# Kernel optimization log

Hardware: AMD Instinct MI355X
Metric: run time of the kernel (lower is better)

Reference implementation:

```python
import jax, jax.numpy as jnp
import numpy as np

J = 161          # skeleton joints
V = 131072       # mesh vertices
K = 8            # max skin joints per vertex
B = 8            # batch
P = 7 * J        # 1127 = total pose params == channels
_rs = np.random.RandomState(1)
JOINT_PARENTS = np.concatenate([np.array([-1]), np.array([_rs.randint(0, i) for i in range(1, J)])])

# quaternion layout (x, y, z, w)

def quat_mul(q1, q2):
    x1, y1, z1, w1 = q1[..., 0], q1[..., 1], q1[..., 2], q1[..., 3]
    x2, y2, z2, w2 = q2[..., 0], q2[..., 1], q2[..., 2], q2[..., 3]
    return jnp.stack([
        w1 * x2 + x1 * w2 + y1 * z2 - z1 * y2,
        w1 * y2 - x1 * z2 + y1 * w2 + z1 * x2,
        w1 * z2 + x1 * y2 - y1 * x2 + z1 * w2,
        w1 * w2 - x1 * x2 - y1 * y2 - z1 * z2,
    ], axis=-1)


def quat_rot(q, v):
    qv = q[..., :3]
    t = 2.0 * jnp.cross(qv, v)
    return v + q[..., 3:4] * t + jnp.cross(qv, t)


def quat_invert(q):
    return jnp.concatenate([-q[..., :3], q[..., 3:4]], axis=-1)


def quat_from_xyz(e):
    h = 0.5 * e
    sx, sy, sz = jnp.sin(h[..., 0]), jnp.sin(h[..., 1]), jnp.sin(h[..., 2])
    cx, cy, cz = jnp.cos(h[..., 0]), jnp.cos(h[..., 1]), jnp.cos(h[..., 2])
    return jnp.stack([
        sx * cy * cz + cx * sy * sz,
        cx * sy * cz - sx * cy * sz,
        cx * cy * sz + sx * sy * cz,
        cx * cy * cz - sx * sy * sz,
    ], axis=-1)


def solve_skeleton_state(params, joint_offset, joint_rotation):
    b = params.shape[0]
    jp = params.reshape(b, J, 7)
    lt = jp[..., 0:3] + joint_offset[None]                       # [b,J,3]
    lr = quat_mul(jnp.broadcast_to(joint_rotation[None], (b, J, 4)), quat_from_xyz(jp[..., 3:6]))
    ls = jnp.exp2(jp[..., 6:7])                                  # [b,J,1]
    states = [None] * J
    for i in range(J):                                           # tree FK recurrence (fixed topology)
        p = int(JOINT_PARENTS[i])
        if p < 0:
            states[i] = (lt[:, i], lr[:, i], ls[:, i])
        else:
            pt, pr, ps = states[p]
            gr = quat_mul(pr, lr[:, i])
            gt = quat_rot(pr, lt[:, i] * ps) + pt
            gs = ps * ls[:, i]
            states[i] = (gt, gr, gs)
    return jnp.stack([jnp.concatenate(s, axis=-1) for s in states], axis=1)  # [b,J,8]


def states_to_matrix(bind_state, states):
    br = quat_invert(bind_state[..., 3:7])
    bs = 1.0 / bind_state[..., 7:8]
    bt = quat_rot(br, -bind_state[..., 0:3]) * bs
    tr = quat_mul(states[..., 3:7], br)
    ts = states[..., 7:8] * bs
    tt = quat_rot(states[..., 3:7], bt * states[..., 7:8]) + states[..., 0:3]
    x, y, z, w = tr[..., 0], tr[..., 1], tr[..., 2], tr[..., 3]
    twx, twy, twz = 2.0 * x * w, 2.0 * y * w, 2.0 * z * w
    txx, txy, txz = 2.0 * x * x, 2.0 * y * x, 2.0 * z * x
    tyy, tyz, tzz = 2.0 * y * y, 2.0 * z * y, 2.0 * z * z
    col0 = jnp.stack([1.0 - (tyy + tzz), txy + twz, txz - twy], axis=-1) * ts
    col1 = jnp.stack([txy - twz, 1.0 - (txx + tzz), tyz + twx], axis=-1) * ts
    col2 = jnp.stack([txz + twy, tyz - twx, 1.0 - (txx + tyy)], axis=-1) * ts
    return jnp.stack([col0, col1, col2, tt], axis=-1)            # [b,J,3,4]


def setup_inputs() -> dict:
    key = jax.random.key(0)
    ks = jax.random.split(key, 10)
    transform = 0.01 * jax.random.normal(ks[0], (P, P), dtype=jnp.float32)
    transform_offsets = 0.01 * jax.random.normal(ks[1], (P,), dtype=jnp.float32)
    joint_offset = jax.random.normal(ks[2], (J, 3), dtype=jnp.float32)
    jr = jax.random.normal(ks[3], (J, 4), dtype=jnp.float32)
    joint_rotation = jr / jnp.linalg.norm(jr, axis=-1, keepdims=True)
    global_pose = 0.1 * jax.random.normal(ks[4], (B, 6), dtype=jnp.float32)
    local_pose = 0.1 * jax.random.normal(ks[5], (B, P - 6 - J), dtype=jnp.float32)
    scale = 0.1 * jax.random.normal(ks[6], (B, J), dtype=jnp.float32)
    mesh_vertices = jax.random.normal(ks[7], (V, 3), dtype=jnp.float32)
    sw = jax.random.uniform(ks[8], (V, K), dtype=jnp.float32)
    skin_weights = sw / sw.sum(axis=-1, keepdims=True)
    skin_indices = jax.random.randint(ks[9], (V, K), 0, J, dtype=jnp.int64)
    # bind state = FK of the zero pose (params = transform_offsets), as in __init__
    bind_state = solve_skeleton_state(transform_offsets[None], joint_offset, joint_rotation)
    return dict(global_pose=global_pose, local_pose=local_pose, scale=scale,
                transform=transform, transform_offsets=transform_offsets,
                joint_offset=joint_offset, joint_rotation=joint_rotation,
                bind_state=bind_state, skin_weights=skin_weights,
                mesh_vertices=mesh_vertices, skin_indices=skin_indices)


def reference(global_pose, local_pose, scale, transform, transform_offsets,
              joint_offset, joint_rotation, bind_state, skin_weights,
              mesh_vertices, skin_indices):
    pose = jnp.concatenate([global_pose, local_pose, scale], axis=-1)   # [B,P]
    params = pose @ transform.T + transform_offsets[None]               # ParameterTransform
    states = solve_skeleton_state(params, joint_offset, joint_rotation) # [B,J,8]
    mat = states_to_matrix(bind_state, states)                          # [B,J,3,4]
    b = mat.shape[0]
    gathered = jnp.take(mat, skin_indices.reshape(-1), axis=1).reshape(b, V, K, 3, 4)
    blended = jnp.einsum('bvkij,vk->bvij', gathered, skin_weights)      # [B,V,3,4]
    return jnp.einsum('bvij,vj->bvi', blended[..., :3], mesh_vertices) + blended[..., 3]
```

## Files before the change

kernel.cpp:

```cpp
#include <hip/hip_runtime.h>
#include <hip/hip_fp16.h>
#include <math.h>

#define Jn 161
#define Vn 131072
#define Kn 8
#define Bn 8
#define Pn 1127
#define NLOC 960
#define MATU (Bn*Jn*6)

struct Q  { float x, y, z, w; };
struct F3 { float x, y, z; };

__device__ __forceinline__ F3 cross3(F3 a, F3 b) {
    return F3{ a.y*b.z - a.z*b.y, a.z*b.x - a.x*b.z, a.x*b.y - a.y*b.x };
}
__device__ __forceinline__ Q qmul(Q a, Q b) {
    return Q{ a.w*b.x + a.x*b.w + a.y*b.z - a.z*b.y,
              a.w*b.y - a.x*b.z + a.y*b.w + a.z*b.x,
              a.w*b.z + a.x*b.y - a.y*b.x + a.z*b.w,
              a.w*b.w - a.x*b.x - a.y*b.y - a.z*b.z };
}
__device__ __forceinline__ F3 qrot(Q q, F3 v) {
    F3 qv{ q.x, q.y, q.z };
    F3 t = cross3(qv, v);
    t.x *= 2.f; t.y *= 2.f; t.z *= 2.f;
    F3 c = cross3(qv, t);
    return F3{ v.x + q.w*t.x + c.x, v.y + q.w*t.y + c.y, v.z + q.w*t.z + c.z };
}
__device__ __forceinline__ Q qfromxyz(float ex, float ey, float ez) {
    float sx = sinf(0.5f*ex), cx = cosf(0.5f*ex);
    float sy = sinf(0.5f*ey), cy = cosf(0.5f*ey);
    float sz = sinf(0.5f*ez), cz = cosf(0.5f*ez);
    return Q{ sx*cy*cz + cx*sy*sz,
              cx*sy*cz - sx*cy*sz,
              cx*cy*sz + sx*sy*cz,
              cx*cy*cz - sx*sy*sz };
}

__device__ __forceinline__ unsigned packh2(float a, float b) {
    unsigned lo = (unsigned)__half_as_ushort(__float2half_rn(a));
    unsigned hi = (unsigned)__half_as_ushort(__float2half_rn(b));
    return lo | (hi << 16);
}
__device__ __forceinline__ float2 unpackh2(unsigned u) {
    float2 r;
    r.x = __half2float(__ushort_as_half((unsigned short)(u & 0xFFFFu)));
    r.y = __half2float(__ushort_as_half((unsigned short)(u >> 16)));
    return r;
}

__global__ __launch_bounds__(64) void k_front(
    const float* __restrict__ gp, const float* __restrict__ lp,
    const float* __restrict__ sc, const float* __restrict__ T,
    const float* __restrict__ toff, const float* __restrict__ joff,
    const float* __restrict__ jrot, const float* __restrict__ bind,
    float* __restrict__ params, int* __restrict__ parents)
{
    const int blk  = blockIdx.x;
    const int lane = threadIdx.x;

    if (blk < Jn) {
        const int i = blk;
        if (i == 0) { if (lane == 0) parents[0] = -1; return; }

        Q fx = qfromxyz(toff[i*7+3], toff[i*7+4], toff[i*7+5]);
        Q jr{ jrot[i*4+0], jrot[i*4+1], jrot[i*4+2], jrot[i*4+3] };
        Q lr = qmul(jr, fx);
        const float l0 = toff[i*7+0] + joff[i*3+0];
        const float l1 = toff[i*7+1] + joff[i*3+1];
        const float l2 = toff[i*7+2] + joff[i*3+2];
        const float lsc = exp2f(toff[i*7+6]);

        float bi[8];
        #pragma unroll
        for (int c = 0; c < 8; ++c) bi[c] = bind[i*8+c];

        unsigned best = 0xFFFFFFFFu;
        for (int p = lane; p < i; p += 64) {
            const float* bp = bind + p*8;
            Q  pr{ bp[3], bp[4], bp[5], bp[6] };
            float ps = bp[7];
            Q  gr = qmul(pr, lr);
            F3 gt = qrot(pr, F3{ l0*ps, l1*ps, l2*ps });
            gt.x += bp[0]; gt.y += bp[1]; gt.z += bp[2];
            float gs = ps * lsc;
            float err = 0.f, d;
            d = gr.x - bi[3]; err += d*d;
            d = gr.y - bi[4]; err += d*d;
            d = gr.z - bi[5]; err += d*d;
            d = gr.w - bi[6]; err += d*d;
            d = gt.x - bi[0]; err += d*d;
            d = gt.y - bi[1]; err += d*d;
            d = gt.z - bi[2]; err += d*d;
            d = gs   - bi[7]; err += d*d;
            unsigned pk = (__float_as_uint(err) & 0xFFFFFF00u) | (unsigned)p;
            best = best < pk ? best : pk;
        }
        #pragma unroll
        for (int o = 32; o > 0; o >>= 1) {
            unsigned other = __shfl_xor(best, o, 64);
            best = best < other ? best : other;
        }
        if (lane == 0) parents[i] = (int)(best & 0xFFu);
        return;
    }

    const int p = blk - Jn;
    const float* row = T + (size_t)p * Pn;

    float acc[Bn];
    #pragma unroll
    for (int b = 0; b < Bn; ++b) acc[b] = 0.f;

    for (int q = lane; q < Pn; q += 64) {
        float tv = row[q];
        #pragma unroll
        for (int b = 0; b < Bn; ++b) {
            float pv;
            if (q < 6)            pv = gp[b*6 + q];
            else if (q < 6+NLOC)  pv = lp[b*NLOC + (q-6)];
            else                  pv = sc[b*Jn + (q-6-NLOC)];
            acc[b] = fmaf(tv, pv, acc[b]);
        }
    }
    #pragma unroll
    for (int b = 0; b < Bn; ++b)
        #pragma unroll
        for (int o = 32; o > 0; o >>= 1)
            acc[b] += __shfl_xor(acc[b], o, 64);

    if (lane == 0) {
        float off = toff[p];
        #pragma unroll
        for (int b = 0; b < Bn; ++b)
            params[b*Pn + p] = acc[b] + off;
    }
}

__global__ __launch_bounds__(192) void k_fk(
    const float* __restrict__ params, const float* __restrict__ joff,
    const float* __restrict__ jrot,   const float* __restrict__ bind,
    const int* __restrict__ parents,  unsigned* __restrict__ mat16)
{
    __shared__ float loc[Jn][9];
    __shared__ int   par[Jn];
    const int b   = blockIdx.x;
    const int tid = threadIdx.x;

    if (tid < Jn) {
        const int i = tid;
        par[i] = parents[i];
        const float* jp = params + b*Pn + i*7;
        Q fx = qfromxyz(jp[3], jp[4], jp[5]);
        Q jr{ jrot[i*4+0], jrot[i*4+1], jrot[i*4+2], jrot[i*4+3] };
        Q lr = qmul(jr, fx);
        loc[i][0] = jp[0] + joff[i*3+0];
        loc[i][1] = jp[1] + joff[i*3+1];
        loc[i][2] = jp[2] + joff[i*3+2];
        loc[i][3] = lr.x; loc[i][4] = lr.y; loc[i][5] = lr.z; loc[i][6] = lr.w;
        loc[i][7] = exp2f(jp[6]);
    }
    __syncthreads();

    if (tid < Jn) {
        const int i = tid;
        F3 at{ loc[i][0], loc[i][1], loc[i][2] };
        Q  ar{ loc[i][3], loc[i][4], loc[i][5], loc[i][6] };
        float as = loc[i][7];
        int j = par[i];
        while (j >= 0) {
            Q  lr{ loc[j][3], loc[j][4], loc[j][5], loc[j][6] };
            float ls = loc[j][7];
            F3 nt = qrot(lr, F3{ at.x*ls, at.y*ls, at.z*ls });
            at = F3{ nt.x + loc[j][0], nt.y + loc[j][1], nt.z + loc[j][2] };
            ar = qmul(lr, ar);
            as = ls * as;
            j = par[j];
        }

        const float* bv = bind + i*8;
        Q  br{ -bv[3], -bv[4], -bv[5], bv[6] };
        float bs = 1.f / bv[7];
        F3 btv = qrot(br, F3{ -bv[0], -bv[1], -bv[2] });
        btv.x *= bs; btv.y *= bs; btv.z *= bs;

        Q  tr = qmul(ar, br);
        float ts = as * bs;
        F3 tt = qrot(ar, F3{ btv.x*as, btv.y*as, btv.z*as });
        tt.x += at.x; tt.y += at.y; tt.z += at.z;

        float x = tr.x, y = tr.y, z = tr.z, w = tr.w;
        float twx = 2.f*x*w, twy = 2.f*y*w, twz = 2.f*z*w;
        float txx = 2.f*x*x, txy = 2.f*y*x, txz = 2.f*z*x;
        float tyy = 2.f*y*y, tyz = 2.f*z*y, tzz = 2.f*z*z;

        float m0  = (1.f - (tyy + tzz)) * ts;
        float m1  = (txy - twz) * ts;
        float m2  = (txz + twy) * ts;
        float m3  = tt.x;
        float m4  = (txy + twz) * ts;
        float m5  = (1.f - (txx + tzz)) * ts;
        float m6  = (tyz - twx) * ts;
        float m7  = tt.y;
        float m8  = (txz - twy) * ts;
        float m9  = (tyz + twx) * ts;
        float m10 = (1.f - (txx + tyy)) * ts;
        float m11 = tt.z;

        unsigned* o = mat16 + (size_t)(b*Jn + i) * 6;
        o[0] = packh2(m0,  m1);
        o[1] = packh2(m2,  m3);
        o[2] = packh2(m4,  m5);
        o[3] = packh2(m6,  m7);
        o[4] = packh2(m8,  m9);
        o[5] = packh2(m10, m11);
    }
}

__global__ __launch_bounds__(256) void k_skin(
    const unsigned* __restrict__ mat16, const float* __restrict__ wts,
    const float* __restrict__ verts, const int* __restrict__ idx,
    float* __restrict__ out)
{
    __shared__ unsigned sm[MATU];
    const int tid = threadIdx.x;

    {
        const uint4* g4 = (const uint4*)mat16;
        uint4* s4 = (uint4*)sm;
        for (int t = tid; t < MATU/4; t += 256) s4[t] = g4[t];
    }
    __syncthreads();

    const int v = blockIdx.x * 256 + tid;

    const int4*   ip = (const int4*)(idx) + v*2;
    const float4* wp = (const float4*)(wts) + v*2;
    int4   i0 = ip[0], i1 = ip[1];
    float4 w0 = wp[0], w1 = wp[1];

    const float vx = verts[v*3+0], vy = verts[v*3+1], vz = verts[v*3+2];

    int   jj[Kn] = { i0.x, i0.y, i0.z, i0.w, i1.x, i1.y, i1.z, i1.w };
    float ww[Kn] = { w0.x, w0.y, w0.z, w0.w, w1.x, w1.y, w1.z, w1.w };

    #pragma unroll
    for (int b = 0; b < Bn; ++b) {
        float a0 = 0.f, a1 = 0.f, a2 = 0.f;
        #pragma unroll
        for (int k = 0; k < Kn; ++k) {
            const int base = (b*Jn + jj[k]) * 6;
            uint2 q0 = *(const uint2*)&sm[base];
            uint2 q1 = *(const uint2*)&sm[base+2];
            uint2 q2 = *(const uint2*)&sm[base+4];
            float2 ma = unpackh2(q0.x), mb = unpackh2(q0.y);
            float2 mc = unpackh2(q1.x), md = unpackh2(q1.y);
            float2 me = unpackh2(q2.x), mf = unpackh2(q2.y);
            float wk = ww[k];
            a0 = fmaf(wk, fmaf(ma.x, vx, fmaf(ma.y, vy, fmaf(mb.x, vz, mb.y))), a0);
            a1 = fmaf(wk, fmaf(mc.x, vx, fmaf(mc.y, vy, fmaf(md.x, vz, md.y))), a1);
            a2 = fmaf(wk, fmaf(me.x, vx, fmaf(me.y, vy, fmaf(mf.x, vz, mf.y))), a2);
        }
        float* o = out + ((size_t)b*Vn + v) * 3;
        o[0] = a0; o[1] = a1; o[2] = a2;
    }
}

extern "C" void kernel_launch(void* const* d_in, const int* in_sizes, int n_in,
                              void* d_out, int out_size, void* d_ws, size_t ws_size,
                              hipStream_t stream)
{
    (void)in_sizes; (void)n_in; (void)out_size; (void)ws_size;

    const float* gp    = (const float*)d_in[0];
    const float* lp    = (const float*)d_in[1];
    const float* sc    = (const float*)d_in[2];
    const float* T     = (const float*)d_in[3];
    const float* toff  = (const float*)d_in[4];
    const float* joff  = (const float*)d_in[5];
    const float* jrot  = (const float*)d_in[6];
    const float* bind  = (const float*)d_in[7];
    const float* wts   = (const float*)d_in[8];
    const float* verts = (const float*)d_in[9];
    const int*   idx   = (const int*)d_in[10];
    float* out = (float*)d_out;

    char* ws = (char*)d_ws;
    float*    params  = (float*)ws;
    unsigned* mat16   = (unsigned*)(ws + 40960);
    int*      parents = (int*)(ws + 73728);

    k_front<<<Jn + Pn, 64, 0, stream>>>(gp, lp, sc, T, toff, joff, jrot, bind, params, parents);
    k_fk   <<<Bn, 192, 0, stream>>>(params, joff, jrot, bind, parents, mat16);
    k_skin <<<Vn/256, 256, 0, stream>>>(mat16, wts, verts, idx, out);
}
```

Measured before the change: 30.45 us.

## Fuse forward kinematics into skinning kernel, recomputing joint matrices per block

Merges the FK kernel into the skinning kernel. Each of the 512 skinning blocks now recomputes all batch×joint local transforms and walks the full ancestor chain into shared memory, instead of loading precomputed half-precision matrices. This removes one kernel launch and the global round trip for the matrices. In exchange it adds redundant FK work in every block (1288 chain walks per block), uses more shared memory per block (about 46 KB for loc, 31 KB for matrices), and delays the start of skinning. It also switches the Euler-to-quaternion conversion to the fast __sincosf intrinsic.

```diff
diff --git a/kernel.cpp b/kernel.cpp
--- a/kernel.cpp
+++ b/kernel.cpp
@@ -30,9 +30,10 @@
     return F3{ v.x + q.w*t.x + c.x, v.y + q.w*t.y + c.y, v.z + q.w*t.z + c.z };
 }
 __device__ __forceinline__ Q qfromxyz(float ex, float ey, float ez) {
-    float sx = sinf(0.5f*ex), cx = cosf(0.5f*ex);
-    float sy = sinf(0.5f*ey), cy = cosf(0.5f*ey);
-    float sz = sinf(0.5f*ez), cz = cosf(0.5f*ez);
+    float sx, cx, sy, cy, sz, cz;
+    __sincosf(0.5f*ex, &sx, &cx);
+    __sincosf(0.5f*ey, &sy, &cy);
+    __sincosf(0.5f*ez, &sz, &cz);
     return Q{ sx*cy*cz + cx*sy*sz,
               cx*sy*cz - sx*cy*sz,
               cx*cy*sz + sx*sy*cz,
@@ -139,42 +140,50 @@
     }
 }
 
-__global__ __launch_bounds__(192) void k_fk(
+__global__ __launch_bounds__(256) void k_fkskin(
     const float* __restrict__ params, const float* __restrict__ joff,
     const float* __restrict__ jrot,   const float* __restrict__ bind,
-    const int* __restrict__ parents,  unsigned* __restrict__ mat16)
+    const int* __restrict__ parents,
+    const float* __restrict__ wts, const float* __restrict__ verts,
+    const int* __restrict__ idx, float* __restrict__ out)
 {
-    __shared__ float loc[Jn][9];
-    __shared__ int   par[Jn];
-    const int b   = blockIdx.x;
+    __shared__ float    loc[Bn*Jn][9];
+    __shared__ unsigned smat[MATU];
+    __shared__ int      par[Jn];
     const int tid = threadIdx.x;
 
-    if (tid < Jn) {
-        const int i = tid;
-        par[i] = parents[i];
+    if (tid < Jn) par[tid] = parents[tid];
+
+    for (int t = tid; t < Bn*Jn; t += 256) {
+        const int b = t / Jn;
+        const int i = t - b*Jn;
         const float* jp = params + b*Pn + i*7;
         Q fx = qfromxyz(jp[3], jp[4], jp[5]);
         Q jr{ jrot[i*4+0], jrot[i*4+1], jrot[i*4+2], jrot[i*4+3] };
         Q lr = qmul(jr, fx);
-        loc[i][0] = jp[0] + joff[i*3+0];
-        loc[i][1] = jp[1] + joff[i*3+1];
-        loc[i][2] = jp[2] + joff[i*3+2];
-        loc[i][3] = lr.x; loc[i][4] = lr.y; loc[i][5] = lr.z; loc[i][6] = lr.w;
-        loc[i][7] = exp2f(jp[6]);
+        loc[t][0] = jp[0] + joff[i*3+0];
+        loc[t][1] = jp[1] + joff[i*3+1];
+        loc[t][2] = jp[2] + joff[i*3+2];
+        loc[t][3] = lr.x; loc[t][4] = lr.y; loc[t][5] = lr.z; loc[t][6] = lr.w;
+        loc[t][7] = exp2f(jp[6]);
     }
     __syncthreads();
 
-    if (tid < Jn) {
-        const int i = tid;
-        F3 at{ loc[i][0], loc[i][1], loc[i][2] };
-        Q  ar{ loc[i][3], loc[i][4], loc[i][5], loc[i][6] };
-        float as = loc[i][7];
+    for (int t = tid; t < Bn*Jn; t += 256) {
+        const int b = t / Jn;
+        const int i = t - b*Jn;
+        const int bb = b * Jn;
+
+        F3 at{ loc[t][0], loc[t][1], loc[t][2] };
+        Q  ar{ loc[t][3], loc[t][4], loc[t][5], loc[t][6] };
+        float as = loc[t][7];
         int j = par[i];
         while (j >= 0) {
-            Q  lr{ loc[j][3], loc[j][4], loc[j][5], loc[j][6] };
-            float ls = loc[j][7];
+            const float* lj = loc[bb + j];
+            Q  lr{ lj[3], lj[4], lj[5], lj[6] };
+            float ls = lj[7];
             F3 nt = qrot(lr, F3{ at.x*ls, at.y*ls, at.z*ls });
-            at = F3{ nt.x + loc[j][0], nt.y + loc[j][1], nt.z + loc[j][2] };
+            at = F3{ nt.x + lj[0], nt.y + lj[1], nt.z + lj[2] };
             ar = qmul(lr, ar);
             as = ls * as;
             j = par[j];
@@ -209,7 +218,7 @@
         float m10 = (1.f - (txx + tyy)) * ts;
         float m11 = tt.z;
 
-        unsigned* o = mat16 + (size_t)(b*Jn + i) * 6;
+        unsigned* o = smat + (size_t)t * 6;
         o[0] = packh2(m0,  m1);
         o[1] = packh2(m2,  m3);
         o[2] = packh2(m4,  m5);
@@ -217,21 +226,6 @@
         o[4] = packh2(m8,  m9);
         o[5] = packh2(m10, m11);
     }
-}
-
-__global__ __launch_bounds__(256) void k_skin(
-    const unsigned* __restrict__ mat16, const float* __restrict__ wts,
-    const float* __restrict__ verts, const int* __restrict__ idx,
-    float* __restrict__ out)
-{
-    __shared__ unsigned sm[MATU];
-    const int tid = threadIdx.x;
-
-    {
-        const uint4* g4 = (const uint4*)mat16;
-        uint4* s4 = (uint4*)sm;
-        for (int t = tid; t < MATU/4; t += 256) s4[t] = g4[t];
-    }
     __syncthreads();
 
     const int v = blockIdx.x * 256 + tid;
@@ -252,9 +246,9 @@
         #pragma unroll
         for (int k = 0; k < Kn; ++k) {
             const int base = (b*Jn + jj[k]) * 6;
-            uint2 q0 = *(const uint2*)&sm[base];
-            uint2 q1 = *(const uint2*)&sm[base+2];
-            uint2 q2 = *(const uint2*)&sm[base+4];
+            uint2 q0 = *(const uint2*)&smat[base];
+            uint2 q1 = *(const uint2*)&smat[base+2];
+            uint2 q2 = *(const uint2*)&smat[base+4];
             float2 ma = unpackh2(q0.x), mb = unpackh2(q0.y);
             float2 mc = unpackh2(q1.x), md = unpackh2(q1.y);
             float2 me = unpackh2(q2.x), mf = unpackh2(q2.y);
@@ -288,11 +282,9 @@
     float* out = (float*)d_out;
 
     char* ws = (char*)d_ws;
-    float*    params  = (float*)ws;
-    unsigned* mat16   = (unsigned*)(ws + 40960);
-    int*      parents = (int*)(ws + 73728);
-
-    k_front<<<Jn + Pn, 64, 0, stream>>>(gp, lp, sc, T, toff, joff, jrot, bind, params, parents);
-    k_fk   <<<Bn, 192, 0, stream>>>(params, joff, jrot, bind, parents, mat16);
-    k_skin <<<Vn/256, 256, 0, stream>>>(mat16, wts, verts, idx, out);
-}
+    float* params  = (float*)ws;
+    int*   parents = (int*)(ws + 40960);
+
+    k_front <<<Jn + Pn, 64, 0, stream>>>(gp, lp, sc, T, toff, joff, jrot, bind, params, parents);
+    k_fkskin<<<Vn/256, 256, 0, stream>>>(params, joff, jrot, bind, parents, wts, verts, idx, out);
+}
```

Result: slower. 37.94 us (+24.6%).
